# Kernel tuning notes

Measured on AMD Instinct MI355X. Metric: run time of the kernel, lower is better.

## Reference

```python
import jax, jax.numpy as jnp
import numpy as np
from jax import lax

B, T, N = 512, 512, 64  # batch, max_seq_len, num_tags


def setup_inputs() -> dict:
    key = jax.random.key(0)
    k1, k2, k3, k4 = jax.random.split(key, 4)
    inputs = jax.random.normal(k1, (B, T, N), dtype=jnp.float32)
    transition_params = jax.random.normal(k2, (N, N), dtype=jnp.float32)
    tag_indices = jax.random.randint(k3, (B, T), 0, N, dtype=jnp.int32)
    sequence_lengths = jax.random.randint(k4, (B,), 0, T, dtype=jnp.int32)
    return {
        "inputs": inputs,
        "transition_params": transition_params,
        "tag_indices": tag_indices,
        "sequence_lengths": sequence_lengths,
    }


def _crf_log_norm(inputs, transition_params, sequence_lengths):
    # inputs: [B, T, N]
    first = inputs[:, 0, :]                       # alpha after first token, [B, N]
    rest = jnp.transpose(inputs[:, 1:, :], (1, 0, 2))  # [T-1, B, N]

    def step(alpha, emit):
        # alpha: [B, N] -> broadcast-add transitions [N, N], logsumexp over prev tag
        new = emit + jax.nn.logsumexp(alpha[:, :, None] + transition_params[None], axis=1)
        return new, new

    _, alphas = lax.scan(step, first, rest)       # [T-1, B, N]
    all_alphas = jnp.concatenate([first[None], alphas], axis=0)  # [T, B, N]
    all_alphas = jnp.transpose(all_alphas, (1, 0, 2))            # [B, T, N]
    last_index = jnp.maximum(0, sequence_lengths - 1)            # [B]
    alpha_last = jnp.take_along_axis(all_alphas, last_index[:, None, None], axis=1)[:, 0, :]
    return jax.nn.logsumexp(alpha_last, axis=1)   # [B]


def _crf_sequence_score(inputs, tag_indices, sequence_lengths, transition_params):
    mask = (jnp.arange(T)[None, :] < sequence_lengths[:, None]).astype(inputs.dtype)  # [B, T]
    # unary: gather emission score of the gold tag at each position
    unary = jnp.take_along_axis(inputs, tag_indices[:, :, None], axis=2)[:, :, 0]      # [B, T]
    unary_scores = jnp.sum(unary * mask, axis=1)
    # binary: transition scores between consecutive gold tags
    binary = transition_params[tag_indices[:, :-1], tag_indices[:, 1:]]                # [B, T-1]
    binary_scores = jnp.sum(binary * mask[:, 1:], axis=1)
    return unary_scores + binary_scores


def reference(inputs, transition_params, tag_indices, sequence_lengths):
    tag_indices = tag_indices.astype(jnp.int32)
    sequence_lengths = sequence_lengths.astype(jnp.int32)
    sequence_scores = _crf_sequence_score(inputs, tag_indices, sequence_lengths, transition_params)
    log_norm = _crf_log_norm(inputs, transition_params, sequence_lengths)
    log_likelihood = sequence_scores - log_norm   # [B]
    return (log_likelihood, transition_params)
```

## Files before the change

kernel.cpp:

```cpp
#include <hip/hip_runtime.h>

#define BB 512
#define TT 512
#define NN 64

__device__ __forceinline__ float readlane_f(float v, int lane) {
    return __int_as_float(__builtin_amdgcn_readlane(__float_as_int(v), lane));
}

__device__ __forceinline__ float dot64(float p, const float4* E) {
    float s0 = readlane_f(p, 0) * E[0].x;
    float s1 = readlane_f(p, 1) * E[0].y;
    float s2 = readlane_f(p, 2) * E[0].z;
    float s3 = readlane_f(p, 3) * E[0].w;
    #pragma unroll
    for (int g = 1; g < 16; ++g) {
        s0 = fmaf(readlane_f(p, 4 * g + 0), E[g].x, s0);
        s1 = fmaf(readlane_f(p, 4 * g + 1), E[g].y, s1);
        s2 = fmaf(readlane_f(p, 4 * g + 2), E[g].z, s2);
        s3 = fmaf(readlane_f(p, 4 * g + 3), E[g].w, s3);
    }
    return (s0 + s1) + (s2 + s3);
}

__global__ __launch_bounds__(64, 1) void crf_kernel(
    const float* __restrict__ inputs,
    const float* __restrict__ trans,
    const int*   __restrict__ tags,
    const int*   __restrict__ lens,
    float*       __restrict__ out)
{
    const int b = blockIdx.x;
    const int j = threadIdx.x;

    if (b < 64) out[BB + b * 64 + j] = trans[b * 64 + j];

    const int L    = lens[b];
    const int last = (L - 1) > 0 ? (L - 1) : 0;

    const float* inb  = inputs + (size_t)b * TT * NN;
    const int*   tagb = tags + (size_t)b * TT;

    float sc = 0.f;
    #pragma unroll
    for (int k = 0; k < 8; ++k) {
        const int t  = k * 64 + j;
        const int tg = tagb[t];
        if (t < L) sc += inb[t * NN + tg];
        if (t + 1 < L) sc += trans[tg * NN + tagb[t + 1]];
    }
    #pragma unroll
    for (int x = 32; x >= 1; x >>= 1) sc += __shfl_xor(sc, x, 64);

    float4 E[16];
    #pragma unroll
    for (int g = 0; g < 16; ++g) {
        E[g].x = __expf(trans[(4 * g + 0) * NN + j]);
        E[g].y = __expf(trans[(4 * g + 1) * NN + j]);
        E[g].z = __expf(trans[(4 * g + 2) * NN + j]);
        E[g].w = __expf(trans[(4 * g + 3) * NN + j]);
    }

    float alpha = inb[j];

    float4 pA0, pA1, pA2, pA3, pB0, pB1, pB2, pB3;

#define LD(vec, comp, tt) { const int tc_ = (tt) <= last ? (tt) : last; \
                            vec.comp = inb[tc_ * NN + j]; }
#define LOADCHUNK(v0, v1, v2, v3, base) \
    LD(v0, x, (base) + 0)  LD(v0, y, (base) + 1)  LD(v0, z, (base) + 2)  LD(v0, w, (base) + 3)  \
    LD(v1, x, (base) + 4)  LD(v1, y, (base) + 5)  LD(v1, z, (base) + 6)  LD(v1, w, (base) + 7)  \
    LD(v2, x, (base) + 8)  LD(v2, y, (base) + 9)  LD(v2, z, (base) + 10) LD(v2, w, (base) + 11) \
    LD(v3, x, (base) + 12) LD(v3, y, (base) + 13) LD(v3, z, (base) + 14) LD(v3, w, (base) + 15)

#define STEP(tc_, EM) { \
    const float m = readlane_f(alpha, 0); \
    const float p = __expf(alpha - m); \
    const float s = dot64(p, E); \
    if ((tc_) <= last) alpha = ((EM) + m) + __logf(s); \
}

    LOADCHUNK(pA0, pA1, pA2, pA3, 1)

    for (int t0 = 1; t0 <= last; t0 += 32) {
        LOADCHUNK(pB0, pB1, pB2, pB3, t0 + 16)
        STEP(t0 + 0,  pA0.x) STEP(t0 + 1,  pA0.y) STEP(t0 + 2,  pA0.z) STEP(t0 + 3,  pA0.w)
        STEP(t0 + 4,  pA1.x) STEP(t0 + 5,  pA1.y) STEP(t0 + 6,  pA1.z) STEP(t0 + 7,  pA1.w)
        STEP(t0 + 8,  pA2.x) STEP(t0 + 9,  pA2.y) STEP(t0 + 10, pA2.z) STEP(t0 + 11, pA2.w)
        STEP(t0 + 12, pA3.x) STEP(t0 + 13, pA3.y) STEP(t0 + 14, pA3.z) STEP(t0 + 15, pA3.w)
        LOADCHUNK(pA0, pA1, pA2, pA3, t0 + 32)
        STEP(t0 + 16, pB0.x) STEP(t0 + 17, pB0.y) STEP(t0 + 18, pB0.z) STEP(t0 + 19, pB0.w)
        STEP(t0 + 20, pB1.x) STEP(t0 + 21, pB1.y) STEP(t0 + 22, pB1.z) STEP(t0 + 23, pB1.w)
        STEP(t0 + 24, pB2.x) STEP(t0 + 25, pB2.y) STEP(t0 + 26, pB2.z) STEP(t0 + 27, pB2.w)
        STEP(t0 + 28, pB3.x) STEP(t0 + 29, pB3.y) STEP(t0 + 30, pB3.z) STEP(t0 + 31, pB3.w)
    }
#undef STEP
#undef LOADCHUNK
#undef LD

    float mm = alpha;
    #pragma unroll
    for (int x = 32; x >= 1; x >>= 1) mm = fmaxf(mm, __shfl_xor(mm, x, 64));
    float e = __expf(alpha - mm);
    #pragma unroll
    for (int x = 32; x >= 1; x >>= 1) e += __shfl_xor(e, x, 64);
    if (j == 0) out[b] = sc - (mm + __logf(e));
}

extern "C" void kernel_launch(void* const* d_in, const int* in_sizes, int n_in,
                              void* d_out, int out_size, void* d_ws, size_t ws_size,
                              hipStream_t stream) {
    const float* inputs = (const float*)d_in[0];
    const float* trans  = (const float*)d_in[1];
    const int*   tags   = (const int*)d_in[2];
    const int*   lens   = (const int*)d_in[3];
    float*       out    = (float*)d_out;

    crf_kernel<<<dim3(BB), dim3(64), 0, stream>>>(inputs, trans, tags, lens, out);
}
```

Baseline: 227.7 us.

## Move exp-transition table to swizzled LDS, batch readlanes in asm, use lagged max

The exponentiated transition matrix moves from 64 per-lane registers into a swizzled shared-memory table, which is reloaded as float4 groups inside each step. The 64 readlane broadcasts are emitted as four inline-asm batches of 16 scalar reads. The stabilizing max now comes from the previous step's alpha lane 0, so the readlane no longer sits between the alpha update and the exp. The aim is to shorten the serial per-step dependency chain. The cost is extra LDS traffic on every recurrence step, and the stale shift could weaken numerical stability if alpha drifts a lot between steps.

```diff
diff --git a/kernel.cpp b/kernel.cpp
--- a/kernel.cpp
+++ b/kernel.cpp
@@ -8,19 +8,32 @@
     return __int_as_float(__builtin_amdgcn_readlane(__float_as_int(v), lane));
 }
 
-__device__ __forceinline__ float dot64(float p, const float4* E) {
-    float s0 = readlane_f(p, 0) * E[0].x;
-    float s1 = readlane_f(p, 1) * E[0].y;
-    float s2 = readlane_f(p, 2) * E[0].z;
-    float s3 = readlane_f(p, 3) * E[0].w;
-    #pragma unroll
-    for (int g = 1; g < 16; ++g) {
-        s0 = fmaf(readlane_f(p, 4 * g + 0), E[g].x, s0);
-        s1 = fmaf(readlane_f(p, 4 * g + 1), E[g].y, s1);
-        s2 = fmaf(readlane_f(p, 4 * g + 2), E[g].z, s2);
-        s3 = fmaf(readlane_f(p, 4 * g + 3), E[g].w, s3);
-    }
-    return (s0 + s1) + (s2 + s3);
+
+#define S2(x) #x
+#define S1(x) S2(x)
+#define RL(o, l) "v_readlane_b32 %" S1(o) ", %16, " S1(l) "\n\t"
+
+#define GRP(G) { \
+    const float4 Fa = ET4[jb + ((4 * (G) + 0) ^ jx)]; \
+    const float4 Fb = ET4[jb + ((4 * (G) + 1) ^ jx)]; \
+    const float4 Fc = ET4[jb + ((4 * (G) + 2) ^ jx)]; \
+    const float4 Fd = ET4[jb + ((4 * (G) + 3) ^ jx)]; \
+    float r0, r1, r2, r3, r4, r5, r6, r7, r8, r9, r10, r11, r12, r13, r14, r15; \
+    asm(RL(0,  (G)*16+0)  RL(1,  (G)*16+1)  RL(2,  (G)*16+2)  RL(3,  (G)*16+3)  \
+        RL(4,  (G)*16+4)  RL(5,  (G)*16+5)  RL(6,  (G)*16+6)  RL(7,  (G)*16+7)  \
+        RL(8,  (G)*16+8)  RL(9,  (G)*16+9)  RL(10, (G)*16+10) RL(11, (G)*16+11) \
+        RL(12, (G)*16+12) RL(13, (G)*16+13) RL(14, (G)*16+14) RL(15, (G)*16+15) \
+        : "=s"(r0), "=s"(r1), "=s"(r2),  "=s"(r3),  "=s"(r4),  "=s"(r5),  "=s"(r6),  "=s"(r7), \
+          "=s"(r8), "=s"(r9), "=s"(r10), "=s"(r11), "=s"(r12), "=s"(r13), "=s"(r14), "=s"(r15) \
+        : "v"(p)); \
+    s0 = fmaf(r0,  Fa.x, s0); s1 = fmaf(r1,  Fa.y, s1); \
+    s2 = fmaf(r2,  Fa.z, s2); s3 = fmaf(r3,  Fa.w, s3); \
+    s0 = fmaf(r4,  Fb.x, s0); s1 = fmaf(r5,  Fb.y, s1); \
+    s2 = fmaf(r6,  Fb.z, s2); s3 = fmaf(r7,  Fb.w, s3); \
+    s0 = fmaf(r8,  Fc.x, s0); s1 = fmaf(r9,  Fc.y, s1); \
+    s2 = fmaf(r10, Fc.z, s2); s3 = fmaf(r11, Fc.w, s3); \
+    s0 = fmaf(r12, Fd.x, s0); s1 = fmaf(r13, Fd.y, s1); \
+    s2 = fmaf(r14, Fd.z, s2); s3 = fmaf(r15, Fd.w, s3); \
 }
 
 __global__ __launch_bounds__(64, 1) void crf_kernel(
@@ -52,16 +65,20 @@
     #pragma unroll
     for (int x = 32; x >= 1; x >>= 1) sc += __shfl_xor(sc, x, 64);
 
-    float4 E[16];
-    #pragma unroll
+    __shared__ __align__(16) float4 ET4[NN * 16];
+    const int jb = j * 16;
+    const int jx = j & 15;
     for (int g = 0; g < 16; ++g) {
-        E[g].x = __expf(trans[(4 * g + 0) * NN + j]);
-        E[g].y = __expf(trans[(4 * g + 1) * NN + j]);
-        E[g].z = __expf(trans[(4 * g + 2) * NN + j]);
-        E[g].w = __expf(trans[(4 * g + 3) * NN + j]);
+        float4 v;
+        v.x = __expf(trans[(4 * g + 0) * NN + j]);
+        v.y = __expf(trans[(4 * g + 1) * NN + j]);
+        v.z = __expf(trans[(4 * g + 2) * NN + j]);
+        v.w = __expf(trans[(4 * g + 3) * NN + j]);
+        ET4[jb + (g ^ jx)] = v;
     }
 
     float alpha = inb[j];
+    float m_sh  = readlane_f(alpha, 0);
 
     float4 pA0, pA1, pA2, pA3, pB0, pB1, pB2, pB3;
 
@@ -74,10 +91,13 @@
     LD(v3, x, (base) + 12) LD(v3, y, (base) + 13) LD(v3, z, (base) + 14) LD(v3, w, (base) + 15)
 
 #define STEP(tc_, EM) { \
-    const float m = readlane_f(alpha, 0); \
-    const float p = __expf(alpha - m); \
-    const float s = dot64(p, E); \
-    if ((tc_) <= last) alpha = ((EM) + m) + __logf(s); \
+    const float mu = m_sh; \
+    const float p  = __expf(alpha - mu); \
+    m_sh = readlane_f(alpha, 0);   \
+    float s0 = 0.f, s1 = 0.f, s2 = 0.f, s3 = 0.f; \
+    GRP(0) GRP(1) GRP(2) GRP(3) \
+    const float s = (s0 + s1) + (s2 + s3); \
+    if ((tc_) <= last) alpha = ((EM) + mu) + __logf(s); \
 }
 
     LOADCHUNK(pA0, pA1, pA2, pA3, 1)
```

Result: no change. 229.6 us (+0.8%).

## Run CRF forward recursion in linear space with power-of-two rescaling and packed FMA asm

Applied to the files above, without the earlier changes.

Replaces the per-step log-space update (max readlane, exp, dot, log) with a linear-domain recursion: alpha is kept as q = exp(alpha - offset), emissions are pre-exponentiated in batches, and each step renormalizes by a power of two taken from lane 0's exponent bits, accumulating the exponent count for the final log. The 64-wide dot product is rewritten in inline asm using scalar readlanes into SGPRs and v_pk_fma_f32 packed FMAs. This removes the transcendental exp/log from the serial critical path and halves the FMA count. In exchange it risks overflow or underflow when emissions or lane 0's value vary widely, relies on hand-written asm with fixed SGPR clobbers and an s_nop hazard guess, and changes the numerics.

```diff
diff --git a/kernel.cpp b/kernel.cpp
--- a/kernel.cpp
+++ b/kernel.cpp
@@ -8,19 +8,66 @@
     return __int_as_float(__builtin_amdgcn_readlane(__float_as_int(v), lane));
 }
 
-__device__ __forceinline__ float dot64(float p, const float4* E) {
-    float s0 = readlane_f(p, 0) * E[0].x;
-    float s1 = readlane_f(p, 1) * E[0].y;
-    float s2 = readlane_f(p, 2) * E[0].z;
-    float s3 = readlane_f(p, 3) * E[0].w;
-    #pragma unroll
-    for (int g = 1; g < 16; ++g) {
-        s0 = fmaf(readlane_f(p, 4 * g + 0), E[g].x, s0);
-        s1 = fmaf(readlane_f(p, 4 * g + 1), E[g].y, s1);
-        s2 = fmaf(readlane_f(p, 4 * g + 2), E[g].z, s2);
-        s3 = fmaf(readlane_f(p, 4 * g + 3), E[g].w, s3);
-    }
-    return (s0 + s1) + (s2 + s3);
+
+#define S2(x) #x
+#define S1(x) S2(x)
+#define RLX(SR, L) "v_readlane_b32 " SR ", %4, " S1(L) "\n\t"
+
+#define SCLOB "s40","s41","s42","s43","s44","s45","s46","s47", \
+              "s48","s49","s50","s51","s52","s53","s54","s55"
+
+#define GRP0() \
+    asm volatile( \
+        "s_nop 4\n\t" \
+        RLX("s40", 0)  RLX("s41", 1)  RLX("s42", 2)  RLX("s43", 3)  \
+        RLX("s44", 4)  RLX("s45", 5)  RLX("s46", 6)  RLX("s47", 7)  \
+        RLX("s48", 8)  RLX("s49", 9)  RLX("s50", 10) RLX("s51", 11) \
+        RLX("s52", 12) RLX("s53", 13) RLX("s54", 14) RLX("s55", 15) \
+        "v_pk_mul_f32 %0, s[40:41], %5\n\t" \
+        "v_pk_mul_f32 %1, s[42:43], %6\n\t" \
+        "v_pk_mul_f32 %2, s[44:45], %7\n\t" \
+        "v_pk_mul_f32 %3, s[46:47], %8\n\t" \
+        "v_pk_fma_f32 %0, s[48:49], %9,  %0\n\t" \
+        "v_pk_fma_f32 %1, s[50:51], %10, %1\n\t" \
+        "v_pk_fma_f32 %2, s[52:53], %11, %2\n\t" \
+        "v_pk_fma_f32 %3, s[54:55], %12, %3\n\t" \
+        : "=&v"(a0), "=&v"(a1), "=&v"(a2), "=&v"(a3) \
+        : "v"(q), \
+          "v"(EP[0]), "v"(EP[1]), "v"(EP[2]), "v"(EP[3]), \
+          "v"(EP[4]), "v"(EP[5]), "v"(EP[6]), "v"(EP[7]) \
+        : SCLOB);
+
+#define GRPN(G) \
+    asm volatile( \
+        RLX("s40", (G)*16+0)  RLX("s41", (G)*16+1)  RLX("s42", (G)*16+2)  RLX("s43", (G)*16+3)  \
+        RLX("s44", (G)*16+4)  RLX("s45", (G)*16+5)  RLX("s46", (G)*16+6)  RLX("s47", (G)*16+7)  \
+        RLX("s48", (G)*16+8)  RLX("s49", (G)*16+9)  RLX("s50", (G)*16+10) RLX("s51", (G)*16+11) \
+        RLX("s52", (G)*16+12) RLX("s53", (G)*16+13) RLX("s54", (G)*16+14) RLX("s55", (G)*16+15) \
+        "v_pk_fma_f32 %0, s[40:41], %5,  %0\n\t" \
+        "v_pk_fma_f32 %1, s[42:43], %6,  %1\n\t" \
+        "v_pk_fma_f32 %2, s[44:45], %7,  %2\n\t" \
+        "v_pk_fma_f32 %3, s[46:47], %8,  %3\n\t" \
+        "v_pk_fma_f32 %0, s[48:49], %9,  %0\n\t" \
+        "v_pk_fma_f32 %1, s[50:51], %10, %1\n\t" \
+        "v_pk_fma_f32 %2, s[52:53], %11, %2\n\t" \
+        "v_pk_fma_f32 %3, s[54:55], %12, %3\n\t" \
+        : "+v"(a0), "+v"(a1), "+v"(a2), "+v"(a3) \
+        : "v"(q), \
+          "v"(EP[8*(G)+0]), "v"(EP[8*(G)+1]), "v"(EP[8*(G)+2]), "v"(EP[8*(G)+3]), \
+          "v"(EP[8*(G)+4]), "v"(EP[8*(G)+5]), "v"(EP[8*(G)+6]), "v"(EP[8*(G)+7]) \
+        : SCLOB);
+
+#define STEP(tc_, EM) { \
+    float2 a0, a1, a2, a3; \
+    GRP0() GRPN(1) GRPN(2) GRPN(3) \
+    const float sdot = ((a0.x + a0.y) + (a1.x + a1.y)) \
+                     + ((a2.x + a2.y) + (a3.x + a3.y)); \
+    const float s0v = readlane_f(sdot, 0); \
+    const int   k   = ((__float_as_int(s0v) >> 23) & 255) - 127; \
+    const bool  act = (tc_) <= last; \
+    kcum += act ? k : 0; \
+    const float qn = (EM) * ldexpf(sdot, -k); \
+    q = act ? qn : q; \
 }
 
 __global__ __launch_bounds__(64, 1) void crf_kernel(
@@ -52,59 +99,53 @@
     #pragma unroll
     for (int x = 32; x >= 1; x >>= 1) sc += __shfl_xor(sc, x, 64);
 
-    float4 E[16];
+    float2 EP[32];
     #pragma unroll
-    for (int g = 0; g < 16; ++g) {
-        E[g].x = __expf(trans[(4 * g + 0) * NN + j]);
-        E[g].y = __expf(trans[(4 * g + 1) * NN + j]);
-        E[g].z = __expf(trans[(4 * g + 2) * NN + j]);
-        E[g].w = __expf(trans[(4 * g + 3) * NN + j]);
+    for (int g = 0; g < 32; ++g) {
+        EP[g].x = __expf(trans[(2 * g)     * NN + j]);
+        EP[g].y = __expf(trans[(2 * g + 1) * NN + j]);
     }
 
-    float alpha = inb[j];
+    const float alpha0 = inb[j];
+    const float m0 = readlane_f(alpha0, 0);
+    float q = __expf(alpha0 - m0);
+    int kcum = 0;
 
-    float4 pA0, pA1, pA2, pA3, pB0, pB1, pB2, pB3;
+    float4 fA0, fA1, fB0, fB1;
 
 #define LD(vec, comp, tt) { const int tc_ = (tt) <= last ? (tt) : last; \
                             vec.comp = inb[tc_ * NN + j]; }
-#define LOADCHUNK(v0, v1, v2, v3, base) \
-    LD(v0, x, (base) + 0)  LD(v0, y, (base) + 1)  LD(v0, z, (base) + 2)  LD(v0, w, (base) + 3)  \
-    LD(v1, x, (base) + 4)  LD(v1, y, (base) + 5)  LD(v1, z, (base) + 6)  LD(v1, w, (base) + 7)  \
-    LD(v2, x, (base) + 8)  LD(v2, y, (base) + 9)  LD(v2, z, (base) + 10) LD(v2, w, (base) + 11) \
-    LD(v3, x, (base) + 12) LD(v3, y, (base) + 13) LD(v3, z, (base) + 14) LD(v3, w, (base) + 15)
+#define LOAD8(v0, v1, base) \
+    LD(v0, x, (base) + 0) LD(v0, y, (base) + 1) LD(v0, z, (base) + 2) LD(v0, w, (base) + 3) \
+    LD(v1, x, (base) + 4) LD(v1, y, (base) + 5) LD(v1, z, (base) + 6) LD(v1, w, (base) + 7)
+#define EXP8(v0, v1) \
+    v0.x = __expf(v0.x); v0.y = __expf(v0.y); v0.z = __expf(v0.z); v0.w = __expf(v0.w); \
+    v1.x = __expf(v1.x); v1.y = __expf(v1.y); v1.z = __expf(v1.z); v1.w = __expf(v1.w);
 
-#define STEP(tc_, EM) { \
-    const float m = readlane_f(alpha, 0); \
-    const float p = __expf(alpha - m); \
-    const float s = dot64(p, E); \
-    if ((tc_) <= last) alpha = ((EM) + m) + __logf(s); \
-}
+    LOAD8(fA0, fA1, 1)
+    EXP8(fA0, fA1)
 
-    LOADCHUNK(pA0, pA1, pA2, pA3, 1)
-
-    for (int t0 = 1; t0 <= last; t0 += 32) {
-        LOADCHUNK(pB0, pB1, pB2, pB3, t0 + 16)
-        STEP(t0 + 0,  pA0.x) STEP(t0 + 1,  pA0.y) STEP(t0 + 2,  pA0.z) STEP(t0 + 3,  pA0.w)
-        STEP(t0 + 4,  pA1.x) STEP(t0 + 5,  pA1.y) STEP(t0 + 6,  pA1.z) STEP(t0 + 7,  pA1.w)
-        STEP(t0 + 8,  pA2.x) STEP(t0 + 9,  pA2.y) STEP(t0 + 10, pA2.z) STEP(t0 + 11, pA2.w)
-        STEP(t0 + 12, pA3.x) STEP(t0 + 13, pA3.y) STEP(t0 + 14, pA3.z) STEP(t0 + 15, pA3.w)
-        LOADCHUNK(pA0, pA1, pA2, pA3, t0 + 32)
-        STEP(t0 + 16, pB0.x) STEP(t0 + 17, pB0.y) STEP(t0 + 18, pB0.z) STEP(t0 + 19, pB0.w)
-        STEP(t0 + 20, pB1.x) STEP(t0 + 21, pB1.y) STEP(t0 + 22, pB1.z) STEP(t0 + 23, pB1.w)
-        STEP(t0 + 24, pB2.x) STEP(t0 + 25, pB2.y) STEP(t0 + 26, pB2.z) STEP(t0 + 27, pB2.w)
-        STEP(t0 + 28, pB3.x) STEP(t0 + 29, pB3.y) STEP(t0 + 30, pB3.z) STEP(t0 + 31, pB3.w)
+    for (int t0 = 1; t0 <= last; t0 += 16) {
+        LOAD8(fB0, fB1, t0 + 8)
+        STEP(t0 + 0, fA0.x) STEP(t0 + 1, fA0.y) STEP(t0 + 2, fA0.z) STEP(t0 + 3, fA0.w)
+        STEP(t0 + 4, fA1.x) STEP(t0 + 5, fA1.y) STEP(t0 + 6, fA1.z) STEP(t0 + 7, fA1.w)
+        EXP8(fB0, fB1)
+        LOAD8(fA0, fA1, t0 + 16)
+        STEP(t0 + 8,  fB0.x) STEP(t0 + 9,  fB0.y) STEP(t0 + 10, fB0.z) STEP(t0 + 11, fB0.w)
+        STEP(t0 + 12, fB1.x) STEP(t0 + 13, fB1.y) STEP(t0 + 14, fB1.z) STEP(t0 + 15, fB1.w)
+        EXP8(fA0, fA1)
     }
-#undef STEP
-#undef LOADCHUNK
+#undef EXP8
+#undef LOAD8
 #undef LD
 
-    float mm = alpha;
+    float qs = q;
     #pragma unroll
-    for (int x = 32; x >= 1; x >>= 1) mm = fmaxf(mm, __shfl_xor(mm, x, 64));
-    float e = __expf(alpha - mm);
-    #pragma unroll
-    for (int x = 32; x >= 1; x >>= 1) e += __shfl_xor(e, x, 64);
-    if (j == 0) out[b] = sc - (mm + __logf(e));
+    for (int x = 32; x >= 1; x >>= 1) qs += __shfl_xor(qs, x, 64);
+    if (j == 0) {
+        const double C = (double)m0 + (double)kcum * 0.6931471805599453;
+        out[b] = sc - (float)((double)__logf(qs) + C);
+    }
 }
 
 extern "C" void kernel_launch(void* const* d_in, const int* in_sizes, int n_in,
```

Measured after the change: 237.6 us. 1.04x slower.
